# Optimization experiments

Hardware: AMD Instinct MI355X
Metric: run time of the kernel (lower is better)

Reference implementation:

```python
import jax, jax.numpy as jnp
import numpy as np

B = 256
NUM_FEATURES = 2048
NUM_MEMORY = 65536
NUM_CLUSTERS = 8000  # static stand-in for labels.max()+1
TEMP = 0.05
EPS_SOFTMAX = 1e-6
EPS_LOG = 1e-6


def setup_inputs() -> dict:
    key = jax.random.key(0)
    k1, k2, k3, k4 = jax.random.split(key, 4)
    results = jax.random.normal(k1, (B, NUM_FEATURES), dtype=jnp.float32)
    indexes = jax.random.randint(k2, (B,), 0, NUM_MEMORY)
    feats = jax.random.normal(k3, (NUM_MEMORY, NUM_FEATURES), dtype=jnp.float32)
    # memory bank rows are L2-normalized in the real module (_update_feature)
    features = feats / jnp.linalg.norm(feats, axis=1, keepdims=True)
    labels = jax.random.randint(k4, (NUM_MEMORY,), 0, NUM_CLUSTERS)
    return {"results": results, "indexes": indexes, "features": features, "labels": labels}


def reference(results, indexes, features, labels):
    # L2-normalize the batch features
    x = results / jnp.linalg.norm(results, axis=1, keepdims=True)  # [B, F]
    # HM.forward: similarity against the full memory bank, scaled by temperature
    logits = jnp.matmul(x, features.T) / TEMP  # [B, M]
    # segment-reduce over memory entries by cluster label (torch index_add_)
    sim = jax.ops.segment_sum(logits.T, labels, num_segments=NUM_CLUSTERS)  # [C, B]
    nums = jax.ops.segment_sum(jnp.ones((NUM_MEMORY,), jnp.float32), labels,
                               num_segments=NUM_CLUSTERS)  # [C]
    mask = nums > 0  # [C] clusters that are populated
    sim = sim / jnp.where(mask, nums, 1.0)[:, None]  # per-cluster mean
    s = sim.T  # [B, C]
    # masked softmax over clusters
    exps = jnp.exp(s) * mask[None, :].astype(s.dtype)
    probs = exps / (jnp.sum(exps, axis=1, keepdims=True) + EPS_SOFTMAX)
    # nll_loss(log(probs + eps), targets)
    targets = labels[indexes]  # [B]
    logp = jnp.log(probs + EPS_LOG)
    return -jnp.mean(logp[jnp.arange(B), targets])
```

## Files before the change

kernel.cpp:

```cpp
#include <hip/hip_runtime.h>
#include <hip/hip_bf16.h>

#define B_ 256
#define F_ 2048
#define M_ 65536
#define C_ 8000
#define TEMP_ 0.05f
#define KSPLIT 4

typedef __attribute__((ext_vector_type(8))) short short8;
typedef __attribute__((ext_vector_type(4))) float f32x4;

__device__ inline unsigned short f2bf(float f) {
  union { float f; unsigned u; } v; v.f = f;
  unsigned r = v.u + 0x7fffu + ((v.u >> 16) & 1u);
  return (unsigned short)(r >> 16);
}

__global__ void k_norm(const float* __restrict__ R, unsigned short* __restrict__ xb,
                       int* __restrict__ counts) {
  int b = blockIdx.x, t = threadIdx.x;
  int g = b * 256 + t;
  if (g < C_) counts[g] = 0;
  const float4* row = (const float4*)(R + (size_t)b * F_);
  float4 v0 = row[t];
  float4 v1 = row[t + 256];
  float ss = v0.x*v0.x + v0.y*v0.y + v0.z*v0.z + v0.w*v0.w
           + v1.x*v1.x + v1.y*v1.y + v1.z*v1.z + v1.w*v1.w;
  __shared__ float red[256];
  red[t] = ss; __syncthreads();
  for (int s = 128; s > 0; s >>= 1) { if (t < s) red[t] += red[t + s]; __syncthreads(); }
  float inv = rsqrtf(red[0]);
  ushort4 o0, o1;
  o0.x = f2bf(v0.x * inv); o0.y = f2bf(v0.y * inv); o0.z = f2bf(v0.z * inv); o0.w = f2bf(v0.w * inv);
  o1.x = f2bf(v1.x * inv); o1.y = f2bf(v1.y * inv); o1.z = f2bf(v1.z * inv); o1.w = f2bf(v1.w * inv);
  ushort4* ob = (ushort4*)(xb + (size_t)b * F_);
  ob[t] = o0; ob[t + 256] = o1;
}

__global__ void k_hist(const int* __restrict__ labels, int* __restrict__ counts) {
  int m = blockIdx.x * 256 + threadIdx.x;
  atomicAdd(&counts[labels[m]], 1);
}

__global__ void k_scan(const int* __restrict__ counts, int* __restrict__ offsets,
                       int* __restrict__ cursor) {
  int t = threadIdx.x;
  int base = t * 32;
  int pre[32];
  int run = 0;
  for (int j = 0; j < 32; j++) {
    int idx = base + j;
    pre[j] = run;
    run += (idx < C_) ? counts[idx] : 0;
  }
  __shared__ int sc[256];
  sc[t] = run; __syncthreads();
  for (int off = 1; off < 256; off <<= 1) {
    int x = (t >= off) ? sc[t - off] : 0;
    __syncthreads();
    sc[t] += x;
    __syncthreads();
  }
  int excl = sc[t] - run;
  for (int j = 0; j < 32; j++) {
    int idx = base + j;
    if (idx < C_) { offsets[idx] = excl + pre[j]; cursor[idx] = 0; }
  }
}

__global__ void k_scatter(const int* __restrict__ labels, const int* __restrict__ offsets,
                          int* __restrict__ cursor, int* __restrict__ order) {
  int m = blockIdx.x * 256 + threadIdx.x;
  int l = labels[m];
  int pos = atomicAdd(&cursor[l], 1);
  order[offsets[l] + pos] = m;
}

__global__ void k_csum(const float* __restrict__ feats, const int* __restrict__ counts,
                       const int* __restrict__ offsets, const int* __restrict__ order,
                       unsigned short* __restrict__ sb) {
  int c = blockIdx.x, t = threadIdx.x;
  int cnt = counts[c], off = offsets[c];
  float4 a0 = {0.f,0.f,0.f,0.f}, a1 = {0.f,0.f,0.f,0.f};
  float4 c0 = {0.f,0.f,0.f,0.f}, c1 = {0.f,0.f,0.f,0.f};
  __shared__ int mlist[256];
  for (int bas = 0; bas < cnt; bas += 256) {
    int n = cnt - bas; if (n > 256) n = 256;
    if (t < n) mlist[t] = order[off + bas + t];
    __syncthreads();
    int i = 0;
    for (; i + 2 <= n; i += 2) {
      const float4* r0 = (const float4*)(feats + (size_t)mlist[i] * F_);
      const float4* r1 = (const float4*)(feats + (size_t)mlist[i + 1] * F_);
      float4 x0 = r0[t], x1 = r0[t + 256];
      float4 y0 = r1[t], y1 = r1[t + 256];
      a0.x += x0.x; a0.y += x0.y; a0.z += x0.z; a0.w += x0.w;
      a1.x += x1.x; a1.y += x1.y; a1.z += x1.z; a1.w += x1.w;
      c0.x += y0.x; c0.y += y0.y; c0.z += y0.z; c0.w += y0.w;
      c1.x += y1.x; c1.y += y1.y; c1.z += y1.z; c1.w += y1.w;
    }
    if (i < n) {
      const float4* r0 = (const float4*)(feats + (size_t)mlist[i] * F_);
      float4 x0 = r0[t], x1 = r0[t + 256];
      a0.x += x0.x; a0.y += x0.y; a0.z += x0.z; a0.w += x0.w;
      a1.x += x1.x; a1.y += x1.y; a1.z += x1.z; a1.w += x1.w;
    }
    __syncthreads();
  }
  a0.x += c0.x; a0.y += c0.y; a0.z += c0.z; a0.w += c0.w;
  a1.x += c1.x; a1.y += c1.y; a1.z += c1.z; a1.w += c1.w;
  float scale = (cnt > 0) ? 1.0f / (TEMP_ * (float)cnt) : 0.0f;
  ushort4 o0, o1;
  o0.x = f2bf(a0.x * scale); o0.y = f2bf(a0.y * scale); o0.z = f2bf(a0.z * scale); o0.w = f2bf(a0.w * scale);
  o1.x = f2bf(a1.x * scale); o1.y = f2bf(a1.y * scale); o1.z = f2bf(a1.z * scale); o1.w = f2bf(a1.w * scale);
  ushort4* ob = (ushort4*)(sb + (size_t)c * F_);
  ob[t] = o0; ob[t + 256] = o1;
}

#define BK 64
#define SK 72

__global__ __launch_bounds__(256) void k_gemm(const unsigned short* __restrict__ xb,
                                              const unsigned short* __restrict__ sb,
                                              float* __restrict__ simp) {
  __shared__ __align__(16) short As[128 * SK];
  __shared__ __align__(16) short Bs[128 * SK];
  int t = threadIdx.x;
  int b0 = blockIdx.x * 128;
  int c0 = blockIdx.y * 128;
  int kz = blockIdx.z;
  int k_begin = kz * (F_ / KSPLIT);
  int k_end = k_begin + (F_ / KSPLIT);
  int wave = t >> 6, lane = t & 63;
  int wr = (wave >> 1) * 64, wc = (wave & 1) * 64;
  int m = lane & 15, q = lane >> 4;
  f32x4 acc[4][4];
  for (int i = 0; i < 4; i++)
    for (int j = 0; j < 4; j++)
      acc[i][j] = (f32x4){0.f, 0.f, 0.f, 0.f};

  for (int kk = k_begin; kk < k_end; kk += BK) {
    __syncthreads();
    for (int i = 0; i < 4; i++) {
      int cid = t + i * 256;
      int row = cid >> 3, cc = cid & 7;
      short8 av = *(const short8*)(xb + (size_t)(b0 + row) * F_ + kk + cc * 8);
      *(short8*)(As + row * SK + cc * 8) = av;
      int gc = c0 + row;
      short8 bv = {0, 0, 0, 0, 0, 0, 0, 0};
      if (gc < C_) bv = *(const short8*)(sb + (size_t)gc * F_ + kk + cc * 8);
      *(short8*)(Bs + row * SK + cc * 8) = bv;
    }
    __syncthreads();
    for (int ks = 0; ks < 2; ks++) {
      int kof = ks * 32 + q * 8;
      short8 af[4], bfr[4];
      for (int i = 0; i < 4; i++)
        af[i] = *(const short8*)(As + (wr + i * 16 + m) * SK + kof);
      for (int j = 0; j < 4; j++)
        bfr[j] = *(const short8*)(Bs + (wc + j * 16 + m) * SK + kof);
      for (int i = 0; i < 4; i++)
        for (int j = 0; j < 4; j++)
          acc[i][j] = __builtin_amdgcn_mfma_f32_16x16x32_bf16(af[i], bfr[j], acc[i][j], 0, 0, 0);
    }
  }
  float* sim = simp + (size_t)kz * B_ * C_;
  for (int i = 0; i < 4; i++) {
    for (int j = 0; j < 4; j++) {
      int col = c0 + wc + j * 16 + m;
      if (col < C_) {
        int rbase = b0 + wr + i * 16 + q * 4;
        f32x4 v = acc[i][j];
        sim[(size_t)(rbase + 0) * C_ + col] = v[0];
        sim[(size_t)(rbase + 1) * C_ + col] = v[1];
        sim[(size_t)(rbase + 2) * C_ + col] = v[2];
        sim[(size_t)(rbase + 3) * C_ + col] = v[3];
      }
    }
  }
}

__global__ void k_loss(const float* __restrict__ simp, const int* __restrict__ counts,
                       const int* __restrict__ labels, const int* __restrict__ indexes,
                       float* __restrict__ lossb) {
  int b = blockIdx.x, t = threadIdx.x;
  int tb = labels[indexes[b]];
  const float* s0 = simp + (size_t)b * C_;
  const float* s1 = s0 + (size_t)B_ * C_;
  const float* s2 = s1 + (size_t)B_ * C_;
  const float* s3 = s2 + (size_t)B_ * C_;
  __shared__ float sst;
  __shared__ float red[256];
  float sum = 0.f;
  for (int c = t; c < C_; c += 256) {
    float v = s0[c] + s1[c] + s2[c] + s3[c];
    float e = (counts[c] > 0) ? __expf(v) : 0.f;
    sum += e;
    if (c == tb) sst = e;
  }
  red[t] = sum; __syncthreads();
  for (int s = 128; s > 0; s >>= 1) { if (t < s) red[t] += red[t + s]; __syncthreads(); }
  if (t == 0) {
    float p = sst / (red[0] + 1e-6f);
    lossb[b] = -logf(p + 1e-6f);
  }
}

__global__ void k_mean(const float* __restrict__ lossb, float* __restrict__ out) {
  int t = threadIdx.x;
  __shared__ float red[256];
  red[t] = lossb[t]; __syncthreads();
  for (int s = 128; s > 0; s >>= 1) { if (t < s) red[t] += red[t + s]; __syncthreads(); }
  if (t == 0) out[0] = red[0] * (1.0f / 256.0f);
}

extern "C" void kernel_launch(void* const* d_in, const int* in_sizes, int n_in,
                              void* d_out, int out_size, void* d_ws, size_t ws_size,
                              hipStream_t stream) {
  const float* results  = (const float*)d_in[0];
  const int*   indexes  = (const int*)d_in[1];
  const float* features = (const float*)d_in[2];
  const int*   labels   = (const int*)d_in[3];
  float* out = (float*)d_out;

  const size_t REQ = (((size_t)B_ * F_ * 2 + 255) & ~(size_t)255)
                   + (((size_t)C_ * F_ * 2 + 255) & ~(size_t)255)
                   + 3 * (((size_t)C_ * 4 + 255) & ~(size_t)255)
                   + (((size_t)M_ * 4 + 255) & ~(size_t)255)
                   + (((size_t)KSPLIT * B_ * C_ * 4 + 255) & ~(size_t)255)
                   + (((size_t)B_ * 4 + 255) & ~(size_t)255);
  if (ws_size < REQ) {
    hipMemsetAsync(d_out, 0, (size_t)out_size * 4, stream);
    return;
  }

  char* p = (char*)d_ws;
  auto carve = [&](size_t bytes) {
    char* r = p;
    p += (bytes + 255) & ~(size_t)255;
    return r;
  };
  unsigned short* xb  = (unsigned short*)carve((size_t)B_ * F_ * 2);
  unsigned short* sbf = (unsigned short*)carve((size_t)C_ * F_ * 2);
  int* counts  = (int*)carve((size_t)C_ * 4);
  int* offsets = (int*)carve((size_t)C_ * 4);
  int* cursor  = (int*)carve((size_t)C_ * 4);
  int* order   = (int*)carve((size_t)M_ * 4);
  float* simp  = (float*)carve((size_t)KSPLIT * B_ * C_ * 4);
  float* lossb = (float*)carve((size_t)B_ * 4);

  k_norm<<<B_, 256, 0, stream>>>(results, xb, counts);
  k_hist<<<M_ / 256, 256, 0, stream>>>(labels, counts);
  k_scan<<<1, 256, 0, stream>>>(counts, offsets, cursor);
  k_scatter<<<M_ / 256, 256, 0, stream>>>(labels, offsets, cursor, order);
  k_csum<<<C_, 256, 0, stream>>>(features, counts, offsets, order, sbf);
  dim3 g(2, 63, KSPLIT);
  k_gemm<<<g, 256, 0, stream>>>(xb, sbf, simp);
  k_loss<<<B_, 256, 0, stream>>>(simp, counts, labels, indexes, lossb);
  k_mean<<<1, 256, 0, stream>>>(lossb, out);
}
```

Before: 777.7 us.

## Fuse masked softmax exp-sum into GEMM epilogue and drop split-K partial buffers

The GEMM no longer uses split-K. It switches to 32x128 tiles over the full K range and computes exp, mask, and per-row partial sums directly in its epilogue. The target numerator is written from the epilogue, so the 4x256x8000 fp32 similarity buffer and the separate loss kernel are removed. This cuts a large amount of global memory traffic and one launch. In exchange, each tile now loops over all of K with small tiles, which lowers MFMA reuse per block and gives 504 blocks in place of 504 split ones.

Result: slower. 808.0 us (+3.9%).

```diff
diff --git a/kernel.cpp b/kernel.cpp
--- a/kernel.cpp
+++ b/kernel.cpp
@@ -6,7 +6,7 @@
 #define M_ 65536
 #define C_ 8000
 #define TEMP_ 0.05f
-#define KSPLIT 4
+#define GW 63
 
 typedef __attribute__((ext_vector_type(8))) short short8;
 typedef __attribute__((ext_vector_type(4))) float f32x4;
@@ -44,8 +44,10 @@
 }
 
 __global__ void k_scan(const int* __restrict__ counts, int* __restrict__ offsets,
-                       int* __restrict__ cursor) {
+                       int* __restrict__ cursor, const int* __restrict__ labels,
+                       const int* __restrict__ indexes, int* __restrict__ tgt) {
   int t = threadIdx.x;
+  tgt[t] = labels[indexes[t]];
   int base = t * 32;
   int pre[32];
   int run = 0;
@@ -123,30 +125,35 @@
 
 __global__ __launch_bounds__(256) void k_gemm(const unsigned short* __restrict__ xb,
                                               const unsigned short* __restrict__ sb,
-                                              float* __restrict__ simp) {
-  __shared__ __align__(16) short As[128 * SK];
+                                              const int* __restrict__ counts,
+                                              const int* __restrict__ tgt,
+                                              float* __restrict__ partials,
+                                              float* __restrict__ tnum) {
+  __shared__ __align__(16) short As[32 * SK];
   __shared__ __align__(16) short Bs[128 * SK];
+  __shared__ float wred[4][32];
+  __shared__ int tgt_l[32];
   int t = threadIdx.x;
-  int b0 = blockIdx.x * 128;
+  int b0 = blockIdx.x * 32;
   int c0 = blockIdx.y * 128;
-  int kz = blockIdx.z;
-  int k_begin = kz * (F_ / KSPLIT);
-  int k_end = k_begin + (F_ / KSPLIT);
+  if (t < 32) tgt_l[t] = tgt[b0 + t];
   int wave = t >> 6, lane = t & 63;
-  int wr = (wave >> 1) * 64, wc = (wave & 1) * 64;
   int m = lane & 15, q = lane >> 4;
-  f32x4 acc[4][4];
-  for (int i = 0; i < 4; i++)
-    for (int j = 0; j < 4; j++)
+  f32x4 acc[2][2];
+  for (int i = 0; i < 2; i++)
+    for (int j = 0; j < 2; j++)
       acc[i][j] = (f32x4){0.f, 0.f, 0.f, 0.f};
 
-  for (int kk = k_begin; kk < k_end; kk += BK) {
-    __syncthreads();
+  for (int kk = 0; kk < F_; kk += BK) {
+    __syncthreads();
+    {
+      int row = t >> 3, cc = t & 7;
+      short8 av = *(const short8*)(xb + (size_t)(b0 + row) * F_ + kk + cc * 8);
+      *(short8*)(As + row * SK + cc * 8) = av;
+    }
     for (int i = 0; i < 4; i++) {
       int cid = t + i * 256;
       int row = cid >> 3, cc = cid & 7;
-      short8 av = *(const short8*)(xb + (size_t)(b0 + row) * F_ + kk + cc * 8);
-      *(short8*)(As + row * SK + cc * 8) = av;
       int gc = c0 + row;
       short8 bv = {0, 0, 0, 0, 0, 0, 0, 0};
       if (gc < C_) bv = *(const short8*)(sb + (size_t)gc * F_ + kk + cc * 8);
@@ -155,63 +162,61 @@
     __syncthreads();
     for (int ks = 0; ks < 2; ks++) {
       int kof = ks * 32 + q * 8;
-      short8 af[4], bfr[4];
-      for (int i = 0; i < 4; i++)
-        af[i] = *(const short8*)(As + (wr + i * 16 + m) * SK + kof);
-      for (int j = 0; j < 4; j++)
-        bfr[j] = *(const short8*)(Bs + (wc + j * 16 + m) * SK + kof);
-      for (int i = 0; i < 4; i++)
-        for (int j = 0; j < 4; j++)
+      short8 af[2], bfr[2];
+      for (int i = 0; i < 2; i++)
+        af[i] = *(const short8*)(As + (i * 16 + m) * SK + kof);
+      for (int j = 0; j < 2; j++)
+        bfr[j] = *(const short8*)(Bs + (wave * 32 + j * 16 + m) * SK + kof);
+      for (int i = 0; i < 2; i++)
+        for (int j = 0; j < 2; j++)
           acc[i][j] = __builtin_amdgcn_mfma_f32_16x16x32_bf16(af[i], bfr[j], acc[i][j], 0, 0, 0);
     }
   }
-  float* sim = simp + (size_t)kz * B_ * C_;
-  for (int i = 0; i < 4; i++) {
-    for (int j = 0; j < 4; j++) {
-      int col = c0 + wc + j * 16 + m;
-      if (col < C_) {
-        int rbase = b0 + wr + i * 16 + q * 4;
-        f32x4 v = acc[i][j];
-        sim[(size_t)(rbase + 0) * C_ + col] = v[0];
-        sim[(size_t)(rbase + 1) * C_ + col] = v[1];
-        sim[(size_t)(rbase + 2) * C_ + col] = v[2];
-        sim[(size_t)(rbase + 3) * C_ + col] = v[3];
+
+  float prow[2][4];
+  for (int i = 0; i < 2; i++)
+    for (int r = 0; r < 4; r++)
+      prow[i][r] = 0.f;
+  for (int j = 0; j < 2; j++) {
+    int col = c0 + wave * 32 + j * 16 + m;
+    bool ok = (col < C_) && (counts[col] > 0);
+    for (int i = 0; i < 2; i++) {
+      f32x4 v = acc[i][j];
+      for (int r = 0; r < 4; r++) {
+        float e = ok ? __expf(v[r]) : 0.f;
+        prow[i][r] += e;
+        int row = i * 16 + q * 4 + r;
+        if (ok && col == tgt_l[row]) tnum[b0 + row] = e;
       }
     }
   }
-}
-
-__global__ void k_loss(const float* __restrict__ simp, const int* __restrict__ counts,
-                       const int* __restrict__ labels, const int* __restrict__ indexes,
-                       float* __restrict__ lossb) {
-  int b = blockIdx.x, t = threadIdx.x;
-  int tb = labels[indexes[b]];
-  const float* s0 = simp + (size_t)b * C_;
-  const float* s1 = s0 + (size_t)B_ * C_;
-  const float* s2 = s1 + (size_t)B_ * C_;
-  const float* s3 = s2 + (size_t)B_ * C_;
-  __shared__ float sst;
+  for (int i = 0; i < 2; i++) {
+    for (int r = 0; r < 4; r++) {
+      float s = prow[i][r];
+      s += __shfl_xor(s, 1);
+      s += __shfl_xor(s, 2);
+      s += __shfl_xor(s, 4);
+      s += __shfl_xor(s, 8);
+      if (m == 0) wred[wave][i * 16 + q * 4 + r] = s;
+    }
+  }
+  __syncthreads();
+  if (t < 32) {
+    float s = wred[0][t] + wred[1][t] + wred[2][t] + wred[3][t];
+    partials[(size_t)blockIdx.y * B_ + b0 + t] = s;
+  }
+}
+
+__global__ void k_final(const float* __restrict__ partials, const float* __restrict__ tnum,
+                        float* __restrict__ out) {
+  int t = threadIdx.x;
+  float s = 0.f;
+  for (int y = 0; y < GW; y++) s += partials[(size_t)y * B_ + t];
+  float p = tnum[t] / (s + 1e-6f);
+  float l = -logf(p + 1e-6f);
   __shared__ float red[256];
-  float sum = 0.f;
-  for (int c = t; c < C_; c += 256) {
-    float v = s0[c] + s1[c] + s2[c] + s3[c];
-    float e = (counts[c] > 0) ? __expf(v) : 0.f;
-    sum += e;
-    if (c == tb) sst = e;
-  }
-  red[t] = sum; __syncthreads();
-  for (int s = 128; s > 0; s >>= 1) { if (t < s) red[t] += red[t + s]; __syncthreads(); }
-  if (t == 0) {
-    float p = sst / (red[0] + 1e-6f);
-    lossb[b] = -logf(p + 1e-6f);
-  }
-}
-
-__global__ void k_mean(const float* __restrict__ lossb, float* __restrict__ out) {
-  int t = threadIdx.x;
-  __shared__ float red[256];
-  red[t] = lossb[t]; __syncthreads();
-  for (int s = 128; s > 0; s >>= 1) { if (t < s) red[t] += red[t + s]; __syncthreads(); }
+  red[t] = l; __syncthreads();
+  for (int st = 128; st > 0; st >>= 1) { if (t < st) red[t] += red[t + st]; __syncthreads(); }
   if (t == 0) out[0] = red[0] * (1.0f / 256.0f);
 }
 
@@ -228,7 +233,8 @@
                    + (((size_t)C_ * F_ * 2 + 255) & ~(size_t)255)
                    + 3 * (((size_t)C_ * 4 + 255) & ~(size_t)255)
                    + (((size_t)M_ * 4 + 255) & ~(size_t)255)
-                   + (((size_t)KSPLIT * B_ * C_ * 4 + 255) & ~(size_t)255)
+                   + (((size_t)B_ * 4 + 255) & ~(size_t)255)
+                   + (((size_t)GW * B_ * 4 + 255) & ~(size_t)255)
                    + (((size_t)B_ * 4 + 255) & ~(size_t)255);
   if (ws_size < REQ) {
     hipMemsetAsync(d_out, 0, (size_t)out_size * 4, stream);
@@ -243,20 +249,20 @@
   };
   unsigned short* xb  = (unsigned short*)carve((size_t)B_ * F_ * 2);
   unsigned short* sbf = (unsigned short*)carve((size_t)C_ * F_ * 2);
-  int* counts  = (int*)carve((size_t)C_ * 4);
-  int* offsets = (int*)carve((size_t)C_ * 4);
-  int* cursor  = (int*)carve((size_t)C_ * 4);
-  int* order   = (int*)carve((size_t)M_ * 4);
-  float* simp  = (float*)carve((size_t)KSPLIT * B_ * C_ * 4);
-  float* lossb = (float*)carve((size_t)B_ * 4);
+  int* counts   = (int*)carve((size_t)C_ * 4);
+  int* offsets  = (int*)carve((size_t)C_ * 4);
+  int* cursor   = (int*)carve((size_t)C_ * 4);
+  int* order    = (int*)carve((size_t)M_ * 4);
+  int* tgt      = (int*)carve((size_t)B_ * 4);
+  float* partials = (float*)carve((size_t)GW * B_ * 4);
+  float* tnum   = (float*)carve((size_t)B_ * 4);
 
   k_norm<<<B_, 256, 0, stream>>>(results, xb, counts);
   k_hist<<<M_ / 256, 256, 0, stream>>>(labels, counts);
-  k_scan<<<1, 256, 0, stream>>>(counts, offsets, cursor);
+  k_scan<<<1, 256, 0, stream>>>(counts, offsets, cursor, labels, indexes, tgt);
   k_scatter<<<M_ / 256, 256, 0, stream>>>(labels, offsets, cursor, order);
   k_csum<<<C_, 256, 0, stream>>>(features, counts, offsets, order, sbf);
-  dim3 g(2, 63, KSPLIT);
-  k_gemm<<<g, 256, 0, stream>>>(xb, sbf, simp);
-  k_loss<<<B_, 256, 0, stream>>>(simp, counts, labels, indexes, lossb);
-  k_mean<<<1, 256, 0, stream>>>(lossb, out);
-}
+  dim3 g(B_ / 32, GW);
+  k_gemm<<<g, 256, 0, stream>>>(xb, sbf, counts, tgt, partials, tnum);
+  k_final<<<1, 256, 0, stream>>>(partials, tnum, out);
+}
```
